# Optimization experiments

Measured on AMD Instinct MI355X. Metric: run time of the kernel, lower is better.

Reference implementation:

```python
import jax, jax.numpy as jnp
import numpy as np

BN_EPS = 1e-5

def _batchnorm(h, gamma, beta):
    # PyTorch BatchNorm1d in training mode: biased batch statistics over dim 0
    mu = jnp.mean(h, axis=0)
    var = jnp.mean((h - mu) ** 2, axis=0)
    return (h - mu) * jax.lax.rsqrt(var + BN_EPS) * gamma + beta


def setup_inputs() -> dict:
    key = jax.random.key(0)
    ks = jax.random.split(key, 8)
    N, E, D = 50000, 800000, 128
    x = jax.random.normal(ks[0], (N, D), dtype=jnp.float32)
    edge_index = jax.random.randint(ks[1], (2, E), 0, N, dtype=jnp.int64)
    s1 = 1.0 / np.sqrt(D)
    W1 = jax.random.uniform(ks[2], (D, D), jnp.float32, -s1, s1)
    b1 = jax.random.uniform(ks[3], (D,), jnp.float32, -s1, s1)
    W2 = jax.random.uniform(ks[4], (D, D), jnp.float32, -s1, s1)
    b2 = jax.random.uniform(ks[5], (D,), jnp.float32, -s1, s1)
    g1 = jnp.ones((D,), jnp.float32); beta1 = jnp.zeros((D,), jnp.float32)
    g2 = jnp.ones((D,), jnp.float32); beta2 = jnp.zeros((D,), jnp.float32)
    eps = jnp.array([0.1], jnp.float32)
    return {"x": x, "edge_index": edge_index, "eps": eps,
            "W1": W1, "b1": b1, "g1": g1, "beta1": beta1,
            "W2": W2, "b2": b2, "g2": g2, "beta2": beta2}


def reference(x, edge_index, eps, W1, b1, g1, beta1, W2, b2, g2, beta2):
    src, dst = edge_index[0], edge_index[1]
    N = x.shape[0]
    # gather by src, scatter-add to dst
    aggr = jax.ops.segment_sum(x[src], dst, num_segments=N)
    out = (1.0 + eps) * x + aggr  # eps broadcast (shape [1])
    h = jax.nn.relu(_batchnorm(out @ W1 + b1, g1, beta1))
    h = jax.nn.relu(_batchnorm(h @ W2 + b2, g2, beta2))
    return h
```

## Files before the change

### kernel.cpp

```cpp
#include <hip/hip_runtime.h>

#define D 128
#define FB 4096
#define GCAP 1024

typedef __attribute__((ext_vector_type(8))) short short8;
typedef __attribute__((ext_vector_type(4))) float f32x4;

static __device__ __forceinline__ unsigned short f2bf(float f) {
    union { float f; unsigned u; } v; v.f = f;
    unsigned r = v.u + 0x7FFF + ((v.u >> 16) & 1);
    return (unsigned short)(r >> 16);
}

static __device__ __forceinline__ float2 bfpair2f(unsigned p) {
    union { unsigned u; float f; } a, b;
    a.u = (p & 0xFFFFu) << 16;
    b.u = p & 0xFFFF0000u;
    return make_float2(a.f, b.f);
}

__global__ __launch_bounds__(256) void prep_kernel(
    const float4* __restrict__ x4, uint2* __restrict__ xh, int xtotal,
    const float* __restrict__ W1, const float* __restrict__ W2,
    unsigned short* __restrict__ Wf1, unsigned short* __restrict__ Wf2,
    float* __restrict__ stats, int* __restrict__ bucketCount,
    unsigned short* __restrict__ zrow, int xblocks)
{
    if (blockIdx.x < (unsigned)xblocks) {
        int i = blockIdx.x * 256 + threadIdx.x;
        if (i >= xtotal) return;
        float4 v = x4[i];
        uint2 o;
        o.x = (unsigned)f2bf(v.x) | ((unsigned)f2bf(v.y) << 16);
        o.y = (unsigned)f2bf(v.z) | ((unsigned)f2bf(v.w) << 16);
        xh[i] = o;
    } else if (blockIdx.x < (unsigned)(xblocks + 128)) {
        int idx = (blockIdx.x - xblocks) * 256 + threadIdx.x;
        const float* W = (idx < 16384) ? W1 : W2;
        unsigned short* Wf = (idx < 16384) ? Wf1 : Wf2;
        int e = idx & 16383;
        int j = e & 7, lane = (e >> 3) & 63, ckk = e >> 9;
        int ct = ckk & 7, kk = ckk >> 3;
        int k = kk * 32 + (lane >> 4) * 8 + j;
        int n = ct * 16 + (lane & 15);
        Wf[e] = f2bf(W[k * 128 + n]);
    } else {
        int t = threadIdx.x;
        stats[t] = 0.f; stats[t + 256] = 0.f;
        bucketCount[t] = 0; bucketCount[t + 256] = 0;
        if (t < 128) zrow[t] = 0;
    }
}

__global__ __launch_bounds__(256) void bucket_hist_kernel(
    const int* __restrict__ ei, int E, int NB, int* __restrict__ bucketCount)
{
    __shared__ int hist[512];
    int tid = threadIdx.x;
    for (int i = tid; i < NB; i += 256) hist[i] = 0;
    __syncthreads();
    int b0 = blockIdx.x * FB;
    int lim = min(FB, E - b0);
    for (int i = tid; i < lim; i += 256)
        atomicAdd(&hist[ei[E + b0 + i] >> 7], 1);
    __syncthreads();
    for (int i = tid; i < NB; i += 256)
        if (hist[i]) atomicAdd(&bucketCount[i], hist[i]);
}

__global__ __launch_bounds__(512) void bucket_scan_kernel(
    const int* __restrict__ bucketCount, int NB, int E,
    int* __restrict__ bucketBase, int* __restrict__ bucketCursor)
{
    __shared__ int sm[512];
    int tid = threadIdx.x;
    int v = (tid < NB) ? bucketCount[tid] : 0;
    sm[tid] = v;
    __syncthreads();
    #pragma unroll
    for (int off = 1; off < 512; off <<= 1) {
        int u = (tid >= off) ? sm[tid - off] : 0;
        __syncthreads();
        sm[tid] += u;
        __syncthreads();
    }
    if (tid < NB) {
        int ex = sm[tid] - v;
        bucketBase[tid] = ex;
        bucketCursor[tid] = ex;
    }
    if (tid == 0) bucketBase[NB] = E;
}

__global__ __launch_bounds__(256) void bucket_fill_kernel(
    const int* __restrict__ ei, int E, int NB,
    int* __restrict__ bucketCursor, unsigned* __restrict__ rec)
{
    __shared__ int hist[512], base[512];
    int tid = threadIdx.x;
    int b0 = blockIdx.x * FB;
    for (int i = tid; i < NB; i += 256) hist[i] = 0;
    __syncthreads();
    int lim = min(FB, E - b0);
    for (int i = tid; i < lim; i += 256)
        atomicAdd(&hist[ei[E + b0 + i] >> 7], 1);
    __syncthreads();
    for (int i = tid; i < NB; i += 256) {
        int c = hist[i];
        base[i] = c ? atomicAdd(&bucketCursor[i], c) : 0;
        hist[i] = 0;
    }
    __syncthreads();
    for (int i = tid; i < lim; i += 256) {
        int e = b0 + i;
        int dst = ei[E + e], src = ei[e];
        int bk = dst >> 7;
        int r = atomicAdd(&hist[bk], 1);
        rec[base[bk] + r] = ((unsigned)src << 7) | (unsigned)(dst & 127);
    }
}

__global__ __launch_bounds__(256) void bucket_gather_kernel(
    const unsigned* __restrict__ xh, const unsigned* __restrict__ rec,
    const int* __restrict__ bucketBase, const float* __restrict__ epsp,
    unsigned* __restrict__ h0, int N, int zrow)
{
    int bk = blockIdx.x >> 2;
    int sub = blockIdx.x & 3;
    int tid = threadIdx.x;
    int d0 = (bk << 7) + (sub << 5);

    __shared__ int cnts[32], rnk[32], offs[33];
    __shared__ int slist[GCAP];

    if (tid < 32) { cnts[tid] = 0; rnk[tid] = 0; }
    __syncthreads();

    int lo = bucketBase[bk], hi = bucketBase[bk + 1];
    for (int i = lo + tid; i < hi; i += 256) {
        unsigned r = rec[i];
        int dl = r & 127;
        if ((dl >> 5) == sub) atomicAdd(&cnts[dl & 31], 1);
    }
    __syncthreads();
    if (tid == 0) {
        int run = 0;
        #pragma unroll
        for (int i = 0; i < 32; ++i) { offs[i] = run; run += cnts[i]; }
        offs[32] = run;
    }
    __syncthreads();
    for (int i = lo + tid; i < hi; i += 256) {
        unsigned r = rec[i];
        int dl = r & 127;
        if ((dl >> 5) == sub) {
            int d5 = dl & 31;
            int rk = atomicAdd(&rnk[d5], 1);
            int pos = offs[d5] + rk;
            if (pos < GCAP) slist[pos] = (int)(r >> 7);
        }
    }
    __syncthreads();

    int wv = tid >> 6, lane = tid & 63;
    float epsv = 1.0f + __ldg(epsp);

    #pragma unroll 1
    for (int jj = 0; jj < 4; ++jj) {
        int dA = d0 + wv * 8 + jj * 2;
        int dB = dA + 1;
        int vA = (dA < N), vB = (dB < N);
        int iA = offs[(dA - d0)];
        int eA = offs[(dA - d0) + 1];
        int iB = vB ? offs[(dB - d0)] : 0;
        int eB = vB ? offs[(dB - d0) + 1] : 0;
        if (iA > GCAP) iA = GCAP;
        if (eA > GCAP) eA = GCAP;
        if (iB > GCAP) iB = GCAP;
        if (eB > GCAP) eB = GCAP;
        if (!vA) { iA = 0; eA = 0; }

        float2 xvA = bfpair2f(xh[(size_t)(vA ? dA : 0) * 64 + lane]);
        float2 xvB = bfpair2f(xh[(size_t)(vB ? dB : 0) * 64 + lane]);
        float axA = epsv * xvA.x, ayA = epsv * xvA.y;
        float axB = epsv * xvB.x, ayB = epsv * xvB.y;

        int iters = (eA - iA) > (eB - iB) ? (eA - iA) : (eB - iB);
        for (int it = 0; it < iters; it += 8) {
            unsigned pvA[8], pvB[8];
            #pragma unroll
            for (int k = 0; k < 8; ++k) {
                int idxA = (iA + k < eA) ? slist[iA + k] : zrow;
                int idxB = (iB + k < eB) ? slist[iB + k] : zrow;
                pvA[k] = xh[(size_t)idxA * 64 + lane];
                pvB[k] = xh[(size_t)idxB * 64 + lane];
            }
            #pragma unroll
            for (int k = 0; k < 8; ++k) {
                float2 a = bfpair2f(pvA[k]);
                float2 b = bfpair2f(pvB[k]);
                axA += a.x; ayA += a.y;
                axB += b.x; ayB += b.y;
            }
            iA += 8; iB += 8;
        }
        if (vA) h0[(size_t)dA * 64 + lane] =
            (unsigned)f2bf(axA) | ((unsigned)f2bf(ayA) << 16);
        if (vB) h0[(size_t)dB * 64 + lane] =
            (unsigned)f2bf(axB) | ((unsigned)f2bf(ayB) << 16);
    }
}

__global__ __launch_bounds__(256) void gemm_bn_mfma_kernel(
    const unsigned short* __restrict__ a_bf,
    const float* __restrict__ stat_in, const float* __restrict__ gamma,
    const float* __restrict__ beta, float invN,
    const unsigned short* __restrict__ Wf, const float* __restrict__ bias,
    unsigned short* __restrict__ zout,
    float* __restrict__ stat_sum, float* __restrict__ stat_sq,
    int N, int mode)
{
    __shared__ unsigned short Wl[16384];
    __shared__ float part[1024];
    __shared__ float scf[128], shf[128];

    int tid = threadIdx.x;
    {
        float4* dst = (float4*)Wl;
        const float4* srcp = (const float4*)Wf;
        #pragma unroll
        for (int i = 0; i < 8; ++i) dst[tid + i * 256] = srcp[tid + i * 256];
    }
    if (mode == 1 && tid < 128) {
        float mean = stat_in[tid] * invN;
        float var  = stat_in[128 + tid] * invN - mean * mean;
        float sv = gamma[tid] * rsqrtf(var + 1e-5f);
        scf[tid] = sv;
        shf[tid] = fmaf(-mean, sv, beta[tid]);
    }
    __syncthreads();

    int w = tid >> 6, lane = tid & 63, q = lane >> 4, n16 = lane & 15;
    int rowb = blockIdx.x * 64 + w * 16;
    int m = rowb + n16;
    int mc = (m < N) ? m : (N - 1);
    const unsigned short* arow = a_bf + (size_t)mc * D;

    f32x4 acc[8];
    #pragma unroll
    for (int ct = 0; ct < 8; ++ct) acc[ct] = (f32x4){0.f, 0.f, 0.f, 0.f};

    #pragma unroll
    for (int kk = 0; kk < 4; ++kk) {
        int c = kk * 32 + q * 8;
        short8 af;
        if (mode == 0) {
            af = *(const short8*)(arow + c);
        } else {
            uint4 rw = *(const uint4*)(arow + c);
            float2 p0 = bfpair2f(rw.x), p1 = bfpair2f(rw.y);
            float2 p2 = bfpair2f(rw.z), p3 = bfpair2f(rw.w);
            p0.x = fmaxf(fmaf(p0.x, scf[c + 0], shf[c + 0]), 0.f);
            p0.y = fmaxf(fmaf(p0.y, scf[c + 1], shf[c + 1]), 0.f);
            p1.x = fmaxf(fmaf(p1.x, scf[c + 2], shf[c + 2]), 0.f);
            p1.y = fmaxf(fmaf(p1.y, scf[c + 3], shf[c + 3]), 0.f);
            p2.x = fmaxf(fmaf(p2.x, scf[c + 4], shf[c + 4]), 0.f);
            p2.y = fmaxf(fmaf(p2.y, scf[c + 5], shf[c + 5]), 0.f);
            p3.x = fmaxf(fmaf(p3.x, scf[c + 6], shf[c + 6]), 0.f);
            p3.y = fmaxf(fmaf(p3.y, scf[c + 7], shf[c + 7]), 0.f);
            af[0] = (short)f2bf(p0.x); af[1] = (short)f2bf(p0.y);
            af[2] = (short)f2bf(p1.x); af[3] = (short)f2bf(p1.y);
            af[4] = (short)f2bf(p2.x); af[5] = (short)f2bf(p2.y);
            af[6] = (short)f2bf(p3.x); af[7] = (short)f2bf(p3.y);
        }
        #pragma unroll
        for (int ct = 0; ct < 8; ++ct) {
            short8 bf = *(const short8*)&Wl[(((kk * 8 + ct) * 64) + lane) * 8];
            acc[ct] = __builtin_amdgcn_mfma_f32_16x16x32_bf16(af, bf, acc[ct], 0, 0, 0);
        }
    }

    #pragma unroll
    for (int ct = 0; ct < 8; ++ct) {
        int col = ct * 16 + n16;
        float bv = __ldg(bias + col);
        float s = 0.f, qs = 0.f;
        #pragma unroll
        for (int reg = 0; reg < 4; ++reg) {
            int row = rowb + q * 4 + reg;
            float v = acc[ct][reg] + bv;
            if (row < N) {
                zout[(size_t)row * D + col] = f2bf(v);
                s += v;
                qs = fmaf(v, v, qs);
            }
        }
        s  += __shfl_xor(s, 16, 64);
        s  += __shfl_xor(s, 32, 64);
        qs += __shfl_xor(qs, 16, 64);
        qs += __shfl_xor(qs, 32, 64);
        if (lane < 16) {
            part[w * 128 + col] = s;
            part[512 + w * 128 + col] = qs;
        }
    }
    __syncthreads();

    if (tid < 128) {
        float s  = part[tid] + part[128 + tid] + part[256 + tid] + part[384 + tid];
        float qq = part[512 + tid] + part[640 + tid] + part[768 + tid] + part[896 + tid];
        atomicAdd(&stat_sum[tid], s);
        atomicAdd(&stat_sq[tid], qq);
    }
}

__global__ __launch_bounds__(256) void bn_relu_kernel(
    const uint2* __restrict__ z2, float4* __restrict__ out,
    const float* __restrict__ stat2, const float* __restrict__ gamma,
    const float* __restrict__ beta, float invN, int total4)
{
    __shared__ float sf[128], tf[128];
    int tid = threadIdx.x;
    if (tid < 128) {
        float mean = stat2[tid] * invN;
        float var  = stat2[128 + tid] * invN - mean * mean;
        float sv = gamma[tid] * rsqrtf(var + 1e-5f);
        sf[tid] = sv;
        tf[tid] = fmaf(-mean, sv, beta[tid]);
    }
    __syncthreads();

    int i = blockIdx.x * 256 + tid;
    if (i >= total4) return;
    uint2 zp = z2[i];
    float2 v01 = bfpair2f(zp.x);
    float2 v23 = bfpair2f(zp.y);
    int c = (i & 31) * 4;
    float4 o;
    o.x = fmaxf(fmaf(v01.x, sf[c + 0], tf[c + 0]), 0.f);
    o.y = fmaxf(fmaf(v01.y, sf[c + 1], tf[c + 1]), 0.f);
    o.z = fmaxf(fmaf(v23.x, sf[c + 2], tf[c + 2]), 0.f);
    o.w = fmaxf(fmaf(v23.y, sf[c + 3], tf[c + 3]), 0.f);
    out[i] = o;
}

extern "C" void kernel_launch(void* const* d_in, const int* in_sizes, int n_in,
                              void* d_out, int out_size, void* d_ws, size_t ws_size,
                              hipStream_t stream)
{
    const float* x   = (const float*)d_in[0];
    const int*   ei  = (const int*)d_in[1];
    const float* eps = (const float*)d_in[2];
    const float* W1  = (const float*)d_in[3];
    const float* b1  = (const float*)d_in[4];
    const float* g1  = (const float*)d_in[5];
    const float* be1 = (const float*)d_in[6];
    const float* W2  = (const float*)d_in[7];
    const float* b2  = (const float*)d_in[8];
    const float* g2  = (const float*)d_in[9];
    const float* be2 = (const float*)d_in[10];

    int N = in_sizes[0] / D;
    int E = in_sizes[1] / 2;
    size_t ND = (size_t)N * D;
    int NB = (N + 127) >> 7;

    unsigned short* xh  = (unsigned short*)d_ws;
    unsigned short* z1  = xh;
    unsigned short* region2 = xh + ND + 128;
    unsigned* rec       = (unsigned*)region2;
    unsigned short* z2  = region2;
    float* stats        = (float*)(region2 + ND);
    int* bucketCount    = (int*)(stats + 512);
    int* bucketBase     = bucketCount + 512;
    int* bucketCursor   = bucketBase + 513;
    unsigned short* Wf1 = (unsigned short*)(bucketCursor + 512);
    unsigned short* Wf2 = Wf1 + 16384;

    float* sum1 = stats + 0,   *sq1 = stats + 128;
    float* sum2 = stats + 256, *sq2 = stats + 384;
    unsigned short* h0 = (unsigned short*)d_out;

    int xtotal = N * 32;
    int xblocks = (xtotal + 255) / 256;
    prep_kernel<<<xblocks + 129, 256, 0, stream>>>(
        (const float4*)x, (uint2*)xh, xtotal, W1, W2, Wf1, Wf2,
        stats, bucketCount, xh + ND, xblocks);

    int fblocks = (E + FB - 1) / FB;
    bucket_hist_kernel<<<fblocks, 256, 0, stream>>>(ei, E, NB, bucketCount);
    bucket_scan_kernel<<<1, 512, 0, stream>>>(bucketCount, NB, E, bucketBase, bucketCursor);
    bucket_fill_kernel<<<fblocks, 256, 0, stream>>>(ei, E, NB, bucketCursor, rec);
    bucket_gather_kernel<<<NB * 4, 256, 0, stream>>>(
        (const unsigned*)xh, rec, bucketBase, eps, (unsigned*)h0, N, N);

    int gblocks = (N + 63) / 64;
    gemm_bn_mfma_kernel<<<gblocks, 256, 0, stream>>>(
        h0, nullptr, nullptr, nullptr, 0.f,
        Wf1, b1, z1, sum1, sq1, N, 0);
    gemm_bn_mfma_kernel<<<gblocks, 256, 0, stream>>>(
        z1, sum1, g1, be1, 1.0f / N,
        Wf2, b2, z2, sum2, sq2, N, 1);
    bn_relu_kernel<<<(N * 32 + 255) / 256, 256, 0, stream>>>(
        (const uint2*)z2, (float4*)d_out, sum2, g2, be2, 1.0f / N, N * 32);
}
```

Before: 225.5 us.

## Split gather into 16-node sub-blocks with 4-way ILP; GEMM does 128 rows per block

The gather kernel now launches 8 blocks per 128-node bucket instead of 4. Each block handles 16 destinations, and each wave processes 4 destinations at once in a single pass rather than looping over pairs. This exposes more memory-level parallelism and more blocks for the latency-bound random gathers, at the cost of scanning each bucket's records twice as many times and a smaller slist capacity. The GEMM kernel now covers 128 rows per block with two accumulator sets. This amortizes the per-block W staging in LDS and reuses each B fragment across two MFMAs, but raises register use.

After: 222.9 us. Within noise of the previous version (-1.2%).

```diff
diff --git a/kernel.cpp b/kernel.cpp
--- a/kernel.cpp
+++ b/kernel.cpp
@@ -2,7 +2,7 @@
 
 #define D 128
 #define FB 4096
-#define GCAP 1024
+#define GCAP 512
 
 typedef __attribute__((ext_vector_type(8))) short short8;
 typedef __attribute__((ext_vector_type(4))) float f32x4;
@@ -126,38 +126,38 @@
     const int* __restrict__ bucketBase, const float* __restrict__ epsp,
     unsigned* __restrict__ h0, int N, int zrow)
 {
-    int bk = blockIdx.x >> 2;
-    int sub = blockIdx.x & 3;
-    int tid = threadIdx.x;
-    int d0 = (bk << 7) + (sub << 5);
-
-    __shared__ int cnts[32], rnk[32], offs[33];
+    int bk = blockIdx.x >> 3;
+    int sub = blockIdx.x & 7;
+    int tid = threadIdx.x;
+    int d0 = (bk << 7) + (sub << 4);
+
+    __shared__ int cnts[16], rnk[16], offs[17];
     __shared__ int slist[GCAP];
 
-    if (tid < 32) { cnts[tid] = 0; rnk[tid] = 0; }
+    if (tid < 16) { cnts[tid] = 0; rnk[tid] = 0; }
     __syncthreads();
 
     int lo = bucketBase[bk], hi = bucketBase[bk + 1];
     for (int i = lo + tid; i < hi; i += 256) {
         unsigned r = rec[i];
         int dl = r & 127;
-        if ((dl >> 5) == sub) atomicAdd(&cnts[dl & 31], 1);
+        if ((dl >> 4) == sub) atomicAdd(&cnts[dl & 15], 1);
     }
     __syncthreads();
     if (tid == 0) {
         int run = 0;
         #pragma unroll
-        for (int i = 0; i < 32; ++i) { offs[i] = run; run += cnts[i]; }
-        offs[32] = run;
+        for (int i = 0; i < 16; ++i) { offs[i] = run; run += cnts[i]; }
+        offs[16] = run;
     }
     __syncthreads();
     for (int i = lo + tid; i < hi; i += 256) {
         unsigned r = rec[i];
         int dl = r & 127;
-        if ((dl >> 5) == sub) {
-            int d5 = dl & 31;
-            int rk = atomicAdd(&rnk[d5], 1);
-            int pos = offs[d5] + rk;
+        if ((dl >> 4) == sub) {
+            int d4 = dl & 15;
+            int rk = atomicAdd(&rnk[d4], 1);
+            int pos = offs[d4] + rk;
             if (pos < GCAP) slist[pos] = (int)(r >> 7);
         }
     }
@@ -166,50 +166,90 @@
     int wv = tid >> 6, lane = tid & 63;
     float epsv = 1.0f + __ldg(epsp);
 
-    #pragma unroll 1
-    for (int jj = 0; jj < 4; ++jj) {
-        int dA = d0 + wv * 8 + jj * 2;
-        int dB = dA + 1;
-        int vA = (dA < N), vB = (dB < N);
-        int iA = offs[(dA - d0)];
-        int eA = offs[(dA - d0) + 1];
-        int iB = vB ? offs[(dB - d0)] : 0;
-        int eB = vB ? offs[(dB - d0) + 1] : 0;
-        if (iA > GCAP) iA = GCAP;
-        if (eA > GCAP) eA = GCAP;
-        if (iB > GCAP) iB = GCAP;
-        if (eB > GCAP) eB = GCAP;
-        if (!vA) { iA = 0; eA = 0; }
-
-        float2 xvA = bfpair2f(xh[(size_t)(vA ? dA : 0) * 64 + lane]);
-        float2 xvB = bfpair2f(xh[(size_t)(vB ? dB : 0) * 64 + lane]);
-        float axA = epsv * xvA.x, ayA = epsv * xvA.y;
-        float axB = epsv * xvB.x, ayB = epsv * xvB.y;
-
-        int iters = (eA - iA) > (eB - iB) ? (eA - iA) : (eB - iB);
-        for (int it = 0; it < iters; it += 8) {
-            unsigned pvA[8], pvB[8];
-            #pragma unroll
-            for (int k = 0; k < 8; ++k) {
-                int idxA = (iA + k < eA) ? slist[iA + k] : zrow;
-                int idxB = (iB + k < eB) ? slist[iB + k] : zrow;
-                pvA[k] = xh[(size_t)idxA * 64 + lane];
-                pvB[k] = xh[(size_t)idxB * 64 + lane];
-            }
-            #pragma unroll
-            for (int k = 0; k < 8; ++k) {
-                float2 a = bfpair2f(pvA[k]);
-                float2 b = bfpair2f(pvB[k]);
-                axA += a.x; ayA += a.y;
-                axB += b.x; ayB += b.y;
-            }
-            iA += 8; iB += 8;
-        }
-        if (vA) h0[(size_t)dA * 64 + lane] =
-            (unsigned)f2bf(axA) | ((unsigned)f2bf(ayA) << 16);
-        if (vB) h0[(size_t)dB * 64 + lane] =
-            (unsigned)f2bf(axB) | ((unsigned)f2bf(ayB) << 16);
-    }
+    int dloc = wv * 4;
+    int dA = d0 + dloc, dB = dA + 1, dC = dA + 2, dD = dA + 3;
+    int vA = (dA < N), vB = (dB < N), vC = (dC < N), vD = (dD < N);
+
+    int iA = offs[dloc + 0], eA = offs[dloc + 1];
+    int iB = offs[dloc + 1], eB = offs[dloc + 2];
+    int iC = offs[dloc + 2], eC = offs[dloc + 3];
+    int iD = offs[dloc + 3], eD = offs[dloc + 4];
+    if (iA > GCAP) iA = GCAP;  if (eA > GCAP) eA = GCAP;
+    if (iB > GCAP) iB = GCAP;  if (eB > GCAP) eB = GCAP;
+    if (iC > GCAP) iC = GCAP;  if (eC > GCAP) eC = GCAP;
+    if (iD > GCAP) iD = GCAP;  if (eD > GCAP) eD = GCAP;
+    if (!vA) { iA = 0; eA = 0; }
+    if (!vB) { iB = 0; eB = 0; }
+    if (!vC) { iC = 0; eC = 0; }
+    if (!vD) { iD = 0; eD = 0; }
+
+    float2 xvA = bfpair2f(xh[(size_t)(vA ? dA : 0) * 64 + lane]);
+    float2 xvB = bfpair2f(xh[(size_t)(vB ? dB : 0) * 64 + lane]);
+    float2 xvC = bfpair2f(xh[(size_t)(vC ? dC : 0) * 64 + lane]);
+    float2 xvD = bfpair2f(xh[(size_t)(vD ? dD : 0) * 64 + lane]);
+    float axA = epsv * xvA.x, ayA = epsv * xvA.y;
+    float axB = epsv * xvB.x, ayB = epsv * xvB.y;
+    float axC = epsv * xvC.x, ayC = epsv * xvC.y;
+    float axD = epsv * xvD.x, ayD = epsv * xvD.y;
+
+    int rA = eA - iA, rB = eB - iB, rC = eC - iC, rD = eD - iD;
+    int iters = max(max(rA, rB), max(rC, rD));
+    for (int it = 0; it < iters; it += 8) {
+        unsigned pA[8], pB[8], pC[8], pD[8];
+        #pragma unroll
+        for (int k = 0; k < 8; ++k) {
+            int idxA = (iA + k < eA) ? slist[iA + k] : zrow;
+            int idxB = (iB + k < eB) ? slist[iB + k] : zrow;
+            int idxC = (iC + k < eC) ? slist[iC + k] : zrow;
+            int idxD = (iD + k < eD) ? slist[iD + k] : zrow;
+            pA[k] = xh[(size_t)idxA * 64 + lane];
+            pB[k] = xh[(size_t)idxB * 64 + lane];
+            pC[k] = xh[(size_t)idxC * 64 + lane];
+            pD[k] = xh[(size_t)idxD * 64 + lane];
+        }
+        #pragma unroll
+        for (int k = 0; k < 8; ++k) {
+            float2 a = bfpair2f(pA[k]);
+            float2 b = bfpair2f(pB[k]);
+            float2 c = bfpair2f(pC[k]);
+            float2 d = bfpair2f(pD[k]);
+            axA += a.x; ayA += a.y;
+            axB += b.x; ayB += b.y;
+            axC += c.x; ayC += c.y;
+            axD += d.x; ayD += d.y;
+        }
+        iA += 8; iB += 8; iC += 8; iD += 8;
+    }
+    if (vA) h0[(size_t)dA * 64 + lane] =
+        (unsigned)f2bf(axA) | ((unsigned)f2bf(ayA) << 16);
+    if (vB) h0[(size_t)dB * 64 + lane] =
+        (unsigned)f2bf(axB) | ((unsigned)f2bf(ayB) << 16);
+    if (vC) h0[(size_t)dC * 64 + lane] =
+        (unsigned)f2bf(axC) | ((unsigned)f2bf(ayC) << 16);
+    if (vD) h0[(size_t)dD * 64 + lane] =
+        (unsigned)f2bf(axD) | ((unsigned)f2bf(ayD) << 16);
+}
+
+static __device__ __forceinline__ short8 bn_relu_pack(
+    const unsigned short* arow, int c, const float* scf, const float* shf)
+{
+    uint4 rw = *(const uint4*)(arow + c);
+    float2 p0 = bfpair2f(rw.x), p1 = bfpair2f(rw.y);
+    float2 p2 = bfpair2f(rw.z), p3 = bfpair2f(rw.w);
+    p0.x = fmaxf(fmaf(p0.x, scf[c + 0], shf[c + 0]), 0.f);
+    p0.y = fmaxf(fmaf(p0.y, scf[c + 1], shf[c + 1]), 0.f);
+    p1.x = fmaxf(fmaf(p1.x, scf[c + 2], shf[c + 2]), 0.f);
+    p1.y = fmaxf(fmaf(p1.y, scf[c + 3], shf[c + 3]), 0.f);
+    p2.x = fmaxf(fmaf(p2.x, scf[c + 4], shf[c + 4]), 0.f);
+    p2.y = fmaxf(fmaf(p2.y, scf[c + 5], shf[c + 5]), 0.f);
+    p3.x = fmaxf(fmaf(p3.x, scf[c + 6], shf[c + 6]), 0.f);
+    p3.y = fmaxf(fmaf(p3.y, scf[c + 7], shf[c + 7]), 0.f);
+    short8 af;
+    af[0] = (short)f2bf(p0.x); af[1] = (short)f2bf(p0.y);
+    af[2] = (short)f2bf(p1.x); af[3] = (short)f2bf(p1.y);
+    af[4] = (short)f2bf(p2.x); af[5] = (short)f2bf(p2.y);
+    af[6] = (short)f2bf(p3.x); af[7] = (short)f2bf(p3.y);
+    return af;
 }
 
 __global__ __launch_bounds__(256) void gemm_bn_mfma_kernel(
@@ -242,42 +282,37 @@
     __syncthreads();
 
     int w = tid >> 6, lane = tid & 63, q = lane >> 4, n16 = lane & 15;
-    int rowb = blockIdx.x * 64 + w * 16;
-    int m = rowb + n16;
-    int mc = (m < N) ? m : (N - 1);
-    const unsigned short* arow = a_bf + (size_t)mc * D;
-
-    f32x4 acc[8];
+    int rowb = blockIdx.x * 128 + w * 16;
+    int m0 = rowb + n16;
+    int m1 = rowb + 64 + n16;
+    int mc0 = (m0 < N) ? m0 : (N - 1);
+    int mc1 = (m1 < N) ? m1 : (N - 1);
+    const unsigned short* arow0 = a_bf + (size_t)mc0 * D;
+    const unsigned short* arow1 = a_bf + (size_t)mc1 * D;
+
+    f32x4 acc0[8], acc1[8];
     #pragma unroll
-    for (int ct = 0; ct < 8; ++ct) acc[ct] = (f32x4){0.f, 0.f, 0.f, 0.f};
+    for (int ct = 0; ct < 8; ++ct) {
+        acc0[ct] = (f32x4){0.f, 0.f, 0.f, 0.f};
+        acc1[ct] = (f32x4){0.f, 0.f, 0.f, 0.f};
+    }
 
     #pragma unroll
     for (int kk = 0; kk < 4; ++kk) {
         int c = kk * 32 + q * 8;
-        short8 af;
+        short8 af0, af1;
         if (mode == 0) {
-            af = *(const short8*)(arow + c);
+            af0 = *(const short8*)(arow0 + c);
+            af1 = *(const short8*)(arow1 + c);
         } else {
-            uint4 rw = *(const uint4*)(arow + c);
-            float2 p0 = bfpair2f(rw.x), p1 = bfpair2f(rw.y);
-            float2 p2 = bfpair2f(rw.z), p3 = bfpair2f(rw.w);
-            p0.x = fmaxf(fmaf(p0.x, scf[c + 0], shf[c + 0]), 0.f);
-            p0.y = fmaxf(fmaf(p0.y, scf[c + 1], shf[c + 1]), 0.f);
-            p1.x = fmaxf(fmaf(p1.x, scf[c + 2], shf[c + 2]), 0.f);
-            p1.y = fmaxf(fmaf(p1.y, scf[c + 3], shf[c + 3]), 0.f);
-            p2.x = fmaxf(fmaf(p2.x, scf[c + 4], shf[c + 4]), 0.f);
-            p2.y = fmaxf(fmaf(p2.y, scf[c + 5], shf[c + 5]), 0.f);
-            p3.x = fmaxf(fmaf(p3.x, scf[c + 6], shf[c + 6]), 0.f);
-            p3.y = fmaxf(fmaf(p3.y, scf[c + 7], shf[c + 7]), 0.f);
-            af[0] = (short)f2bf(p0.x); af[1] = (short)f2bf(p0.y);
-            af[2] = (short)f2bf(p1.x); af[3] = (short)f2bf(p1.y);
-            af[4] = (short)f2bf(p2.x); af[5] = (short)f2bf(p2.y);
-            af[6] = (short)f2bf(p3.x); af[7] = (short)f2bf(p3.y);
+            af0 = bn_relu_pack(arow0, c, scf, shf);
+            af1 = bn_relu_pack(arow1, c, scf, shf);
         }
         #pragma unroll
         for (int ct = 0; ct < 8; ++ct) {
             short8 bf = *(const short8*)&Wl[(((kk * 8 + ct) * 64) + lane) * 8];
-            acc[ct] = __builtin_amdgcn_mfma_f32_16x16x32_bf16(af, bf, acc[ct], 0, 0, 0);
+            acc0[ct] = __builtin_amdgcn_mfma_f32_16x16x32_bf16(af0, bf, acc0[ct], 0, 0, 0);
+            acc1[ct] = __builtin_amdgcn_mfma_f32_16x16x32_bf16(af1, bf, acc1[ct], 0, 0, 0);
         }
     }
 
@@ -289,7 +324,17 @@
         #pragma unroll
         for (int reg = 0; reg < 4; ++reg) {
             int row = rowb + q * 4 + reg;
-            float v = acc[ct][reg] + bv;
+            float v = acc0[ct][reg] + bv;
+            if (row < N) {
+                zout[(size_t)row * D + col] = f2bf(v);
+                s += v;
+                qs = fmaf(v, v, qs);
+            }
+        }
+        #pragma unroll
+        for (int reg = 0; reg < 4; ++reg) {
+            int row = rowb + 64 + q * 4 + reg;
+            float v = acc1[ct][reg] + bv;
             if (row < N) {
                 zout[(size_t)row * D + col] = f2bf(v);
                 s += v;
@@ -392,10 +437,10 @@
     bucket_hist_kernel<<<fblocks, 256, 0, stream>>>(ei, E, NB, bucketCount);
     bucket_scan_kernel<<<1, 512, 0, stream>>>(bucketCount, NB, E, bucketBase, bucketCursor);
     bucket_fill_kernel<<<fblocks, 256, 0, stream>>>(ei, E, NB, bucketCursor, rec);
-    bucket_gather_kernel<<<NB * 4, 256, 0, stream>>>(
+    bucket_gather_kernel<<<NB * 8, 256, 0, stream>>>(
         (const unsigned*)xh, rec, bucketBase, eps, (unsigned*)h0, N, N);
 
-    int gblocks = (N + 63) / 64;
+    int gblocks = (N + 127) / 128;
     gemm_bn_mfma_kernel<<<gblocks, 256, 0, stream>>>(
         h0, nullptr, nullptr, nullptr, 0.f,
         Wf1, b1, z1, sum1, sq1, N, 0);
```
